# Optimization experiments

Measured on AMD Instinct MI355X. Metric: run time of the kernel, lower is better.

## Reference

```python
import jax, jax.numpy as jnp
import numpy as np
import math

B, S, D, H = 2, 2048, 1024, 16
HD = D // H  # head_dim = 64


def setup_inputs() -> dict:
    rng = jax.random.key(0)
    ks = jax.random.split(rng, 11)
    std = 1.0 / math.sqrt(D)
    inp = {
        "query": jax.random.normal(ks[0], (B, S, D), dtype=jnp.float32),
        "key": jax.random.normal(ks[1], (B, S, D), dtype=jnp.float32),
        "value": jax.random.normal(ks[2], (B, S, D), dtype=jnp.float32),
        # causal mask: True = masked (ignored), matching masked_fill semantics
        "mask": jnp.triu(jnp.ones((S, S), dtype=bool), k=1),
        "wq": jax.random.normal(ks[3], (D, D), dtype=jnp.float32) * std,
        "bq": jnp.zeros((D,), dtype=jnp.float32),
        "wk": jax.random.normal(ks[4], (D, D), dtype=jnp.float32) * std,
        "bk": jnp.zeros((D,), dtype=jnp.float32),
        "wv": jax.random.normal(ks[5], (D, D), dtype=jnp.float32) * std,
        "bv": jnp.zeros((D,), dtype=jnp.float32),
        "wo": jax.random.normal(ks[6], (D, D), dtype=jnp.float32) * std,
        "bo": jnp.zeros((D,), dtype=jnp.float32),
    }
    return inp


def reference(query, key, value, mask, wq, bq, wk, bk, wv, bv, wo, bo):
    # Linear projections (torch Linear: x @ W.T + b)
    q = jnp.einsum('bsd,ed->bse', query, wq) + bq
    k = jnp.einsum('bsd,ed->bse', key, wk) + bk
    v = jnp.einsum('bsd,ed->bse', value, wv) + bv
    # split heads: (B, S, D) -> (B, H, S, HD)
    q = q.reshape(B, S, H, HD).transpose(0, 2, 1, 3)
    k = k.reshape(B, S, H, HD).transpose(0, 2, 1, 3)
    v = v.reshape(B, S, H, HD).transpose(0, 2, 1, 3)
    # naive attention: materialize full (B, H, Sq, Sk) scores
    scores = jnp.einsum('bhqd,bhkd->bhqk', q, k) / jnp.sqrt(jnp.float32(HD))
    scores = jnp.where(mask[None, None, :, :], -jnp.inf, scores)
    attn = jax.nn.softmax(scores, axis=-1)
    out = jnp.einsum('bhqk,bhkd->bhqd', attn, v)
    out = out.transpose(0, 2, 1, 3).reshape(B, S, D)
    return jnp.einsum('bsd,ed->bse', out, wo) + bo
```

## Files before the change

kernel.cpp:

```cpp
#include <hip/hip_runtime.h>
#include <stdint.h>

#define B_ 2
#define S_ 2048
#define D_ 1024
#define H_ 16
#define HD_ 64
#define M_TOT (B_*S_)

typedef __bf16 bf16;
typedef bf16 bf16x8 __attribute__((ext_vector_type(8)));
typedef float f32x4 __attribute__((ext_vector_type(4)));
typedef float f32x16 __attribute__((ext_vector_type(16)));
typedef unsigned int u32;
typedef unsigned int u32x4v __attribute__((ext_vector_type(4)));

__device__ __forceinline__ void gload_lds16(const void* g, void* l) {
    __builtin_amdgcn_global_load_lds((const __attribute__((address_space(1))) void*)g,
                                     (__attribute__((address_space(3))) void*)l, 16, 0, 0);
}

__device__ __forceinline__ u32 cvtpk_bf16(float lo, float hi) {
    u32 d;
    asm("v_cvt_pk_bf16_f32 %0, %1, %2" : "=v"(d) : "v"(lo), "v"(hi));
    return d;
}

__global__ __launch_bounds__(256) void cvt_kernel(
    const float* __restrict__ q, const float* __restrict__ k, const float* __restrict__ v,
    const float* __restrict__ wq, const float* __restrict__ wk,
    const float* __restrict__ wv, const float* __restrict__ wo,
    bf16* __restrict__ xq, bf16* __restrict__ xk, bf16* __restrict__ xv,
    bf16* __restrict__ wqb, bf16* __restrict__ wkb, bf16* __restrict__ wvb, bf16* __restrict__ wob)
{
    const float* src; bf16* dst; int n;
    switch (blockIdx.y) {
        case 0: src=q;  dst=xq;  n=M_TOT*D_; break;
        case 1: src=k;  dst=xk;  n=M_TOT*D_; break;
        case 2: src=v;  dst=xv;  n=M_TOT*D_; break;
        case 3: src=wq; dst=wqb; n=D_*D_;    break;
        case 4: src=wk; dst=wkb; n=D_*D_;    break;
        case 5: src=wv; dst=wvb; n=D_*D_;    break;
        default: src=wo; dst=wob; n=D_*D_;   break;
    }
    int i = (blockIdx.x*blockDim.x + threadIdx.x)*8;
    if (i >= n) return;
    const f32x4* s4 = (const f32x4*)(src + i);
    f32x4 a = s4[0], b = s4[1];
    bf16x8 o;
    #pragma unroll
    for (int j = 0; j < 4; ++j) { o[j] = (bf16)a[j]; o[j+4] = (bf16)b[j]; }
    *(bf16x8*)(dst + i) = o;
}

__device__ __forceinline__ void gemm_mainloop(const bf16* __restrict__ A, const bf16* __restrict__ Wt,
                                              int brow, int bcol, bf16* As, bf16* Bs,
                                              f32x4 (&acc)[4][4])
{
    const int tid = threadIdx.x;
    const int l = tid & 63, w = tid >> 6;
    const int wr = w >> 1, wc = w & 1;
    const int lr = l & 15, lq = l >> 4;

    for (int k0 = 0; k0 < D_; k0 += 32) {
        #pragma unroll
        for (int i = 0; i < 2; ++i) {
            int id = i*256 + tid;
            int row = id >> 2, c8 = (id & 3) << 3;
            gload_lds16(A  + (size_t)(brow + row)*D_ + k0 + c8, As + id*8);
            gload_lds16(Wt + (size_t)(bcol + row)*D_ + k0 + c8, Bs + id*8);
        }
        __syncthreads();
        bf16x8 af[4], bf[4];
        #pragma unroll
        for (int m = 0; m < 4; ++m)
            af[m] = *(const bf16x8*)&As[(wr*64 + m*16 + lr)*32 + lq*8];
        #pragma unroll
        for (int n = 0; n < 4; ++n)
            bf[n] = *(const bf16x8*)&Bs[(wc*64 + n*16 + lr)*32 + lq*8];
        #pragma unroll
        for (int m = 0; m < 4; ++m)
            #pragma unroll
            for (int n = 0; n < 4; ++n)
                acc[m][n] = __builtin_amdgcn_mfma_f32_16x16x32_bf16(af[m], bf[n], acc[m][n], 0, 0, 0);
        __syncthreads();
    }
}

__global__ __launch_bounds__(256) void gemm_qkv(
    const bf16* __restrict__ xq, const bf16* __restrict__ xk, const bf16* __restrict__ xv,
    const bf16* __restrict__ wqb, const bf16* __restrict__ wkb, const bf16* __restrict__ wvb,
    const float* __restrict__ bq, const float* __restrict__ bk, const float* __restrict__ bv,
    bf16* __restrict__ Qf, bf16* __restrict__ Kf, bf16* __restrict__ Vf)
{
    __shared__ __align__(16) bf16 As[128*32];
    __shared__ __align__(16) bf16 Bs[128*32];
    const int z = blockIdx.z;
    const bf16* A  = (z==0) ? xq  : (z==1) ? xk  : xv;
    const bf16* Wt = (z==0) ? wqb : (z==1) ? wkb : wvb;
    const float* bias = (z==0) ? bq : (z==1) ? bk : bv;

    const int brow = (blockIdx.x & 31)*128;
    const int bcol = (blockIdx.x >> 5)*128;

    f32x4 acc[4][4] = {};
    gemm_mainloop(A, Wt, brow, bcol, As, Bs, acc);

    const int tid = threadIdx.x;
    const int l = tid & 63, w = tid >> 6;
    const int wr = w >> 1, wc = w & 1;
    const int lr = l & 15, lq = l >> 4;

    #pragma unroll
    for (int m = 0; m < 4; ++m)
        #pragma unroll
        for (int n = 0; n < 4; ++n) {
            int col = bcol + wc*64 + n*16 + lr;
            float bv_ = bias[col];
            int h = col >> 6, hd = col & 63;
            #pragma unroll
            for (int r = 0; r < 4; ++r) {
                int row = brow + wr*64 + m*16 + lq*4 + r;
                int b = row >> 11, s = row & 2047;
                float val = acc[m][n][r] + bv_;
                if (z == 0) val *= 0.18033688011112042f;
                size_t hbase = ((size_t)b*H_ + h)*S_*HD_;
                if (z < 2) {
                    int chunk = ((s >> 5) << 2) + (hd >> 4);
                    int lane  = (((hd >> 3) & 1) << 5) | (s & 31);
                    bf16* dst = (z==0) ? Qf : Kf;
                    dst[hbase + (size_t)chunk*512 + lane*8 + (hd & 7)] = (bf16)val;
                } else {
                    int chunk = ((s >> 6) << 3) + (((s >> 4) & 3) << 1) + (hd >> 5);
                    int lane  = (((s >> 3) & 1) << 5) | (hd & 31);
                    Vf[hbase + (size_t)chunk*512 + lane*8 + (s & 7)] = (bf16)val;
                }
            }
        }
}

__global__ __launch_bounds__(256) void gemm_out(
    const bf16* __restrict__ Oat, const bf16* __restrict__ wob,
    const float* __restrict__ bo, float* __restrict__ out)
{
    __shared__ __align__(16) bf16 As[128*32];
    __shared__ __align__(16) bf16 Bs[128*32];
    const int brow = (blockIdx.x & 31)*128;
    const int bcol = (blockIdx.x >> 5)*128;

    f32x4 acc[4][4] = {};
    gemm_mainloop(Oat, wob, brow, bcol, As, Bs, acc);

    const int tid = threadIdx.x;
    const int l = tid & 63, w = tid >> 6;
    const int wr = w >> 1, wc = w & 1;
    const int lr = l & 15, lq = l >> 4;

    #pragma unroll
    for (int m = 0; m < 4; ++m)
        #pragma unroll
        for (int n = 0; n < 4; ++n) {
            int col = bcol + wc*64 + n*16 + lr;
            float bv_ = bo[col];
            #pragma unroll
            for (int r = 0; r < 4; ++r) {
                int row = brow + wr*64 + m*16 + lq*4 + r;
                out[(size_t)row*D_ + col] = acc[m][n][r] + bv_;
            }
        }
}

__global__ __launch_bounds__(64, 2) void attn_kernel(
    const bf16* __restrict__ Qf, const bf16* __restrict__ Kf,
    const bf16* __restrict__ Vf, bf16* __restrict__ Oat)
{
    __shared__ __align__(16) char Osm[32*128];

    const int l = threadIdx.x & 63;
    const int l31 = l & 31, hi = l >> 5;

    const int id = (int)blockIdx.x;
    const int xcd = id & 7, slot = id >> 3;
    const int bh  = xcd + 8*(slot >> 6);
    const int qt  = 63 - (slot & 63);
    const int b = bh >> 4, h = bh & 15;
    const int q0 = qt*32;
    const int qrow = q0 + l31;

    const bf16* Qfp = Qf + (size_t)bh*S_*HD_;
    const bf16* Kfp = Kf + (size_t)bh*S_*HD_;
    const bf16* Vfp = Vf + (size_t)bh*S_*HD_;
    const int l8 = l*8;

    bf16x8 qb[4];
    #pragma unroll
    for (int dc = 0; dc < 4; ++dc)
        qb[dc] = *(const bf16x8*)(Qfp + (size_t)(((q0 >> 5) << 2) + dc)*512 + l8);

    f32x16 ot0 = {}, ot1 = {};
    float mrun = -1e30f, lrun = 0.f;
    const int nkt = q0/64 + 1;

    bf16x8 ka[2][4];
    #pragma unroll
    for (int kv2 = 0; kv2 < 2; ++kv2)
        #pragma unroll
        for (int dc = 0; dc < 4; ++dc)
            ka[kv2][dc] = *(const bf16x8*)(Kfp + (size_t)(kv2*4 + dc)*512 + l8);

    for (int kt = 0; kt < nkt; ++kt) {
        const int kc0 = kt*64;
        const bool last = (kt == nkt - 1);

        const int ktn = (kt + 1 < nkt) ? kt + 1 : kt;
        bf16x8 kn[2][4];
        #pragma unroll
        for (int kv2 = 0; kv2 < 2; ++kv2)
            #pragma unroll
            for (int dc = 0; dc < 4; ++dc)
                kn[kv2][dc] = *(const bf16x8*)(Kfp + (size_t)((ktn*2 + kv2)*4 + dc)*512 + l8);
        bf16x8 va0[4], va1[4];
        #pragma unroll
        for (int c = 0; c < 4; ++c) {
            va0[c] = *(const bf16x8*)(Vfp + (size_t)(kt*8 + c*2 + 0)*512 + l8);
            va1[c] = *(const bf16x8*)(Vfp + (size_t)(kt*8 + c*2 + 1)*512 + l8);
        }

        f32x16 ct0 = {}, ct1 = {};
        #pragma unroll
        for (int dc = 0; dc < 4; ++dc)
            ct0 = __builtin_amdgcn_mfma_f32_32x32x16_bf16(ka[0][dc], qb[dc], ct0, 0, 0, 0);
        #pragma unroll
        for (int dc = 0; dc < 4; ++dc)
            ct1 = __builtin_amdgcn_mfma_f32_32x32x16_bf16(ka[1][dc], qb[dc], ct1, 0, 0, 0);

        if (last) {
            #pragma unroll
            for (int reg = 0; reg < 16; ++reg) {
                const int rr = (reg & 3) + 8*(reg >> 2) + 4*hi;
                if (kc0 + rr > qrow)      ct0[reg] = -1e30f;
                if (kc0 + 32 + rr > qrow) ct1[reg] = -1e30f;
            }
        }

        float t8[8];
        #pragma unroll
        for (int i = 0; i < 8; ++i)
            t8[i] = fmaxf(fmaxf(ct0[i], ct0[i+8]), fmaxf(ct1[i], ct1[i+8]));
        float t4a = fmaxf(t8[0], t8[4]), t4b = fmaxf(t8[1], t8[5]);
        float t4c = fmaxf(t8[2], t8[6]), t4d = fmaxf(t8[3], t8[7]);
        float vm = fmaxf(fmaxf(t4a, t4b), fmaxf(t4c, t4d));
        vm = fmaxf(vm, __shfl_xor(vm, 32));

        if (!__all(vm <= mrun + 8.f)) {
            float nm = fmaxf(mrun, vm);
            float al = exp2f(mrun - nm);
            #pragma unroll
            for (int i = 0; i < 16; ++i) { ot0[i] *= al; ot1[i] *= al; }
            lrun *= al;
            mrun = nm;
        }

        #pragma unroll
        for (int i = 0; i < 16; ++i) {
            ct0[i] = exp2f(ct0[i] - mrun);
            ct1[i] = exp2f(ct1[i] - mrun);
        }
        float s8[8];
        #pragma unroll
        for (int i = 0; i < 8; ++i)
            s8[i] = (ct0[i] + ct0[i+8]) + (ct1[i] + ct1[i+8]);
        float s4a = s8[0]+s8[4], s4b = s8[1]+s8[5], s4c = s8[2]+s8[6], s4d = s8[3]+s8[7];
        float ps = (s4a + s4b) + (s4c + s4d);
        ps += __shfl_xor(ps, 32);
        lrun += ps;

        u32 own0[8], own1[8], oth0[8], oth1[8];
        #pragma unroll
        for (int u = 0; u < 8; ++u) {
            own0[u] = cvtpk_bf16(ct0[2*u], ct0[2*u+1]);
            own1[u] = cvtpk_bf16(ct1[2*u], ct1[2*u+1]);
        }
        #pragma unroll
        for (int u = 0; u < 8; ++u) {
            oth0[u] = __shfl_xor(own0[u], 32);
            oth1[u] = __shfl_xor(own1[u], 32);
        }

        #pragma unroll
        for (int c = 0; c < 4; ++c) {
            const int b0 = 4*(c & 1);
            const u32* Ho = (c >> 1) ? own1 : own0;
            const u32* Hx = (c >> 1) ? oth1 : oth0;
            u32 w0 = hi ? Hx[b0+2] : Ho[b0];
            u32 w1 = hi ? Hx[b0+3] : Ho[b0+1];
            u32 w2 = hi ? Ho[b0+2] : Hx[b0];
            u32 w3 = hi ? Ho[b0+3] : Hx[b0+1];
            u32x4v pw = { w0, w1, w2, w3 };
            bf16x8 pb = __builtin_bit_cast(bf16x8, pw);
            ot0 = __builtin_amdgcn_mfma_f32_32x32x16_bf16(va0[c], pb, ot0, 0, 0, 0);
            ot1 = __builtin_amdgcn_mfma_f32_32x32x16_bf16(va1[c], pb, ot1, 0, 0, 0);
        }

        #pragma unroll
        for (int kv2 = 0; kv2 < 2; ++kv2)
            #pragma unroll
            for (int dc = 0; dc < 4; ++dc)
                ka[kv2][dc] = kn[kv2][dc];
    }

    const float inv = 1.f / lrun;
    #pragma unroll
    for (int rp = 0; rp < 16; rp += 2) {
        const int d0 = (rp & 3) + 8*(rp >> 2) + 4*hi;
        u32 p0 = cvtpk_bf16(ot0[rp]*inv, ot0[rp+1]*inv);
        u32 p1 = cvtpk_bf16(ot1[rp]*inv, ot1[rp+1]*inv);
        const int swz = (l31 & 7) << 4;
        *(u32*)(Osm + l31*128 + (( d0*2)        ^ swz)) = p0;
        *(u32*)(Osm + l31*128 + (((32 + d0)*2)  ^ swz)) = p1;
    }
    #pragma unroll
    for (int p = 0; p < 4; ++p) {
        const int row  = p*8 + (l >> 3);
        const int colb = (l & 7)*16;
        u32x4v v = *(const u32x4v*)(Osm + row*128 + (colb ^ ((row & 7) << 4)));
        char* gp = (char*)Oat + (((size_t)(b*S_ + q0 + row)*D_ + h*64)*2) + colb;
        *(u32x4v*)gp = v;
    }
}

extern "C" void kernel_launch(void* const* d_in, const int* in_sizes, int n_in,
                              void* d_out, int out_size, void* d_ws, size_t ws_size,
                              hipStream_t stream) {
    const float* q  = (const float*)d_in[0];
    const float* k  = (const float*)d_in[1];
    const float* v  = (const float*)d_in[2];
    const float* wq = (const float*)d_in[4];
    const float* bq = (const float*)d_in[5];
    const float* wk = (const float*)d_in[6];
    const float* bk = (const float*)d_in[7];
    const float* wv = (const float*)d_in[8];
    const float* bv = (const float*)d_in[9];
    const float* wo = (const float*)d_in[10];
    const float* bo = (const float*)d_in[11];
    float* out = (float*)d_out;

    char* p = (char*)d_ws;
    const size_t XSZ = (size_t)M_TOT*D_*sizeof(bf16);
    const size_t WSZ = (size_t)D_*D_*sizeof(bf16);
    bf16* xq  = (bf16*)p; p += XSZ;
    bf16* xk  = (bf16*)p; p += XSZ;
    bf16* xv  = (bf16*)p; p += XSZ;
    bf16* wqb = (bf16*)p; p += WSZ;
    bf16* wkb = (bf16*)p; p += WSZ;
    bf16* wvb = (bf16*)p; p += WSZ;
    bf16* wob = (bf16*)p; p += WSZ;
    bf16* Qf  = (bf16*)p; p += XSZ;
    bf16* Kf  = (bf16*)p; p += XSZ;
    bf16* Vf  = (bf16*)p; p += XSZ;
    bf16* Oat = (bf16*)p; p += XSZ;

    cvt_kernel<<<dim3(2048, 7), 256, 0, stream>>>(q, k, v, wq, wk, wv, wo,
                                                  xq, xk, xv, wqb, wkb, wvb, wob);
    gemm_qkv<<<dim3(256, 1, 3), 256, 0, stream>>>(xq, xk, xv, wqb, wkb, wvb,
                                                  bq, bk, bv, Qf, Kf, Vf);
    attn_kernel<<<2048, 64, 0, stream>>>(Qf, Kf, Vf, Oat);
    gemm_out<<<dim3(256), 256, 0, stream>>>(Oat, wob, bo, out);
}
```

Before: 140.3 us.

## Unroll attention KV loop by two with ping-pong K registers and reorder q-tile schedule

The attention key loop is manually unrolled by two through a macro, alternating two K register buffers so the prefetched next tile does not need a copy back into the current buffer. P-fragment selection is rewritten with explicit branches instead of pointer selection, which helps keep the arrays in registers. The q-tile to block mapping is also changed: the causal tile order is interleaved and half the slots run in ascending order, which mixes long and short blocks within each scheduling group. Both K buffers are live at once, which may raise register pressure, and the new block order could change L2 locality.

```diff
diff --git a/kernel.cpp b/kernel.cpp
--- a/kernel.cpp
+++ b/kernel.cpp
@@ -170,6 +170,98 @@
         }
 }
 
+#define ATTN_BODY(CUR, NXT, KT) do {                                                        \
+    const int kc0_ = (KT)*64;                                                               \
+    const bool last_ = ((KT) == nkt - 1);                                                   \
+    const int ktn_ = ((KT) + 1 < nkt) ? (KT) + 1 : (KT);                                    \
+    _Pragma("unroll")                                                                       \
+    for (int kv2 = 0; kv2 < 2; ++kv2)                                                       \
+        _Pragma("unroll")                                                                   \
+        for (int dc = 0; dc < 4; ++dc)                                                      \
+            NXT[kv2][dc] = *(const bf16x8*)(Kfp + (size_t)((ktn_*2 + kv2)*4 + dc)*512 + l8);\
+    bf16x8 va0[4], va1[4];                                                                  \
+    _Pragma("unroll")                                                                       \
+    for (int c = 0; c < 4; ++c) {                                                           \
+        va0[c] = *(const bf16x8*)(Vfp + (size_t)((KT)*8 + c*2 + 0)*512 + l8);               \
+        va1[c] = *(const bf16x8*)(Vfp + (size_t)((KT)*8 + c*2 + 1)*512 + l8);               \
+    }                                                                                       \
+    f32x16 ct0 = {}, ct1 = {};                                                              \
+    _Pragma("unroll")                                                                       \
+    for (int dc = 0; dc < 4; ++dc)                                                          \
+        ct0 = __builtin_amdgcn_mfma_f32_32x32x16_bf16(CUR[0][dc], qb[dc], ct0, 0, 0, 0);    \
+    _Pragma("unroll")                                                                       \
+    for (int dc = 0; dc < 4; ++dc)                                                          \
+        ct1 = __builtin_amdgcn_mfma_f32_32x32x16_bf16(CUR[1][dc], qb[dc], ct1, 0, 0, 0);    \
+    if (last_) {                                                                            \
+        _Pragma("unroll")                                                                   \
+        for (int reg = 0; reg < 16; ++reg) {                                                \
+            const int rr = (reg & 3) + 8*(reg >> 2) + 4*hi;                                 \
+            if (kc0_ + rr > qrow)      ct0[reg] = -1e30f;                                   \
+            if (kc0_ + 32 + rr > qrow) ct1[reg] = -1e30f;                                   \
+        }                                                                                   \
+    }                                                                                       \
+    float t8[8];                                                                            \
+    _Pragma("unroll")                                                                       \
+    for (int i = 0; i < 8; ++i)                                                             \
+        t8[i] = fmaxf(fmaxf(ct0[i], ct0[i+8]), fmaxf(ct1[i], ct1[i+8]));                    \
+    float t4a = fmaxf(t8[0], t8[4]), t4b = fmaxf(t8[1], t8[5]);                             \
+    float t4c = fmaxf(t8[2], t8[6]), t4d = fmaxf(t8[3], t8[7]);                             \
+    float vm = fmaxf(fmaxf(t4a, t4b), fmaxf(t4c, t4d));                                     \
+    vm = fmaxf(vm, __shfl_xor(vm, 32));                                                     \
+    if (!__all(vm <= mrun + 8.f)) {                                                         \
+        float nm = fmaxf(mrun, vm);                                                         \
+        float al = exp2f(mrun - nm);                                                        \
+        _Pragma("unroll")                                                                   \
+        for (int i = 0; i < 16; ++i) { ot0[i] *= al; ot1[i] *= al; }                        \
+        lrun *= al;                                                                         \
+        mrun = nm;                                                                          \
+    }                                                                                       \
+    _Pragma("unroll")                                                                       \
+    for (int i = 0; i < 16; ++i) {                                                          \
+        ct0[i] = exp2f(ct0[i] - mrun);                                                      \
+        ct1[i] = exp2f(ct1[i] - mrun);                                                      \
+    }                                                                                       \
+    float s8[8];                                                                            \
+    _Pragma("unroll")                                                                       \
+    for (int i = 0; i < 8; ++i)                                                             \
+        s8[i] = (ct0[i] + ct0[i+8]) + (ct1[i] + ct1[i+8]);                                  \
+    float s4a = s8[0]+s8[4], s4b = s8[1]+s8[5], s4c = s8[2]+s8[6], s4d = s8[3]+s8[7];       \
+    float ps = (s4a + s4b) + (s4c + s4d);                                                   \
+    ps += __shfl_xor(ps, 32);                                                               \
+    lrun += ps;                                                                             \
+    u32 own0[8], own1[8], oth0[8], oth1[8];                                                 \
+    _Pragma("unroll")                                                                       \
+    for (int u = 0; u < 8; ++u) {                                                           \
+        own0[u] = cvtpk_bf16(ct0[2*u], ct0[2*u+1]);                                         \
+        own1[u] = cvtpk_bf16(ct1[2*u], ct1[2*u+1]);                                         \
+    }                                                                                       \
+    _Pragma("unroll")                                                                       \
+    for (int u = 0; u < 8; ++u) {                                                           \
+        oth0[u] = __shfl_xor(own0[u], 32);                                                  \
+        oth1[u] = __shfl_xor(own1[u], 32);                                                  \
+    }                                                                                       \
+    _Pragma("unroll")                                                                       \
+    for (int c = 0; c < 4; ++c) {                                                           \
+        const int b0 = 4*(c & 1);                                                           \
+        u32 o0, o1, o2, o3, x0, x1, x2, x3;                                                 \
+        if ((c >> 1) == 0) {                                                                \
+            o0 = own0[b0]; o1 = own0[b0+1]; o2 = own0[b0+2]; o3 = own0[b0+3];               \
+            x0 = oth0[b0]; x1 = oth0[b0+1]; x2 = oth0[b0+2]; x3 = oth0[b0+3];               \
+        } else {                                                                            \
+            o0 = own1[b0]; o1 = own1[b0+1]; o2 = own1[b0+2]; o3 = own1[b0+3];               \
+            x0 = oth1[b0]; x1 = oth1[b0+1]; x2 = oth1[b0+2]; x3 = oth1[b0+3];               \
+        }                                                                                   \
+        u32 w0 = hi ? x2 : o0;                                                              \
+        u32 w1 = hi ? x3 : o1;                                                              \
+        u32 w2 = hi ? o2 : x0;                                                              \
+        u32 w3 = hi ? o3 : x1;                                                              \
+        u32x4v pw = { w0, w1, w2, w3 };                                                     \
+        bf16x8 pb = __builtin_bit_cast(bf16x8, pw);                                         \
+        ot0 = __builtin_amdgcn_mfma_f32_32x32x16_bf16(va0[c], pb, ot0, 0, 0, 0);            \
+        ot1 = __builtin_amdgcn_mfma_f32_32x32x16_bf16(va1[c], pb, ot1, 0, 0, 0);            \
+    }                                                                                       \
+} while (0)
+
 __global__ __launch_bounds__(64, 2) void attn_kernel(
     const bf16* __restrict__ Qf, const bf16* __restrict__ Kf,
     const bf16* __restrict__ Vf, bf16* __restrict__ Oat)
@@ -182,7 +274,10 @@
     const int id = (int)blockIdx.x;
     const int xcd = id & 7, slot = id >> 3;
     const int bh  = xcd + 8*(slot >> 6);
-    const int qt  = 63 - (slot & 63);
+    const int s6 = slot & 63;
+    const int sb = s6 & 31;
+    const int g  = ((sb & 7) << 3) | (sb >> 3);
+    const int qt = (s6 < 32) ? g : 63 - g;
     const int b = bh >> 4, h = bh & 15;
     const int q0 = qt*32;
     const int qrow = q0 + l31;
@@ -201,112 +296,20 @@
     float mrun = -1e30f, lrun = 0.f;
     const int nkt = q0/64 + 1;
 
-    bf16x8 ka[2][4];
+    bf16x8 ka[2][4], kb[2][4];
     #pragma unroll
     for (int kv2 = 0; kv2 < 2; ++kv2)
         #pragma unroll
         for (int dc = 0; dc < 4; ++dc)
             ka[kv2][dc] = *(const bf16x8*)(Kfp + (size_t)(kv2*4 + dc)*512 + l8);
 
-    for (int kt = 0; kt < nkt; ++kt) {
-        const int kc0 = kt*64;
-        const bool last = (kt == nkt - 1);
-
-        const int ktn = (kt + 1 < nkt) ? kt + 1 : kt;
-        bf16x8 kn[2][4];
-        #pragma unroll
-        for (int kv2 = 0; kv2 < 2; ++kv2)
-            #pragma unroll
-            for (int dc = 0; dc < 4; ++dc)
-                kn[kv2][dc] = *(const bf16x8*)(Kfp + (size_t)((ktn*2 + kv2)*4 + dc)*512 + l8);
-        bf16x8 va0[4], va1[4];
-        #pragma unroll
-        for (int c = 0; c < 4; ++c) {
-            va0[c] = *(const bf16x8*)(Vfp + (size_t)(kt*8 + c*2 + 0)*512 + l8);
-            va1[c] = *(const bf16x8*)(Vfp + (size_t)(kt*8 + c*2 + 1)*512 + l8);
-        }
-
-        f32x16 ct0 = {}, ct1 = {};
-        #pragma unroll
-        for (int dc = 0; dc < 4; ++dc)
-            ct0 = __builtin_amdgcn_mfma_f32_32x32x16_bf16(ka[0][dc], qb[dc], ct0, 0, 0, 0);
-        #pragma unroll
-        for (int dc = 0; dc < 4; ++dc)
-            ct1 = __builtin_amdgcn_mfma_f32_32x32x16_bf16(ka[1][dc], qb[dc], ct1, 0, 0, 0);
-
-        if (last) {
-            #pragma unroll
-            for (int reg = 0; reg < 16; ++reg) {
-                const int rr = (reg & 3) + 8*(reg >> 2) + 4*hi;
-                if (kc0 + rr > qrow)      ct0[reg] = -1e30f;
-                if (kc0 + 32 + rr > qrow) ct1[reg] = -1e30f;
-            }
-        }
-
-        float t8[8];
-        #pragma unroll
-        for (int i = 0; i < 8; ++i)
-            t8[i] = fmaxf(fmaxf(ct0[i], ct0[i+8]), fmaxf(ct1[i], ct1[i+8]));
-        float t4a = fmaxf(t8[0], t8[4]), t4b = fmaxf(t8[1], t8[5]);
-        float t4c = fmaxf(t8[2], t8[6]), t4d = fmaxf(t8[3], t8[7]);
-        float vm = fmaxf(fmaxf(t4a, t4b), fmaxf(t4c, t4d));
-        vm = fmaxf(vm, __shfl_xor(vm, 32));
-
-        if (!__all(vm <= mrun + 8.f)) {
-            float nm = fmaxf(mrun, vm);
-            float al = exp2f(mrun - nm);
-            #pragma unroll
-            for (int i = 0; i < 16; ++i) { ot0[i] *= al; ot1[i] *= al; }
-            lrun *= al;
-            mrun = nm;
-        }
-
-        #pragma unroll
-        for (int i = 0; i < 16; ++i) {
-            ct0[i] = exp2f(ct0[i] - mrun);
-            ct1[i] = exp2f(ct1[i] - mrun);
-        }
-        float s8[8];
-        #pragma unroll
-        for (int i = 0; i < 8; ++i)
-            s8[i] = (ct0[i] + ct0[i+8]) + (ct1[i] + ct1[i+8]);
-        float s4a = s8[0]+s8[4], s4b = s8[1]+s8[5], s4c = s8[2]+s8[6], s4d = s8[3]+s8[7];
-        float ps = (s4a + s4b) + (s4c + s4d);
-        ps += __shfl_xor(ps, 32);
-        lrun += ps;
-
-        u32 own0[8], own1[8], oth0[8], oth1[8];
-        #pragma unroll
-        for (int u = 0; u < 8; ++u) {
-            own0[u] = cvtpk_bf16(ct0[2*u], ct0[2*u+1]);
-            own1[u] = cvtpk_bf16(ct1[2*u], ct1[2*u+1]);
-        }
-        #pragma unroll
-        for (int u = 0; u < 8; ++u) {
-            oth0[u] = __shfl_xor(own0[u], 32);
-            oth1[u] = __shfl_xor(own1[u], 32);
-        }
-
-        #pragma unroll
-        for (int c = 0; c < 4; ++c) {
-            const int b0 = 4*(c & 1);
-            const u32* Ho = (c >> 1) ? own1 : own0;
-            const u32* Hx = (c >> 1) ? oth1 : oth0;
-            u32 w0 = hi ? Hx[b0+2] : Ho[b0];
-            u32 w1 = hi ? Hx[b0+3] : Ho[b0+1];
-            u32 w2 = hi ? Ho[b0+2] : Hx[b0];
-            u32 w3 = hi ? Ho[b0+3] : Hx[b0+1];
-            u32x4v pw = { w0, w1, w2, w3 };
-            bf16x8 pb = __builtin_bit_cast(bf16x8, pw);
-            ot0 = __builtin_amdgcn_mfma_f32_32x32x16_bf16(va0[c], pb, ot0, 0, 0, 0);
-            ot1 = __builtin_amdgcn_mfma_f32_32x32x16_bf16(va1[c], pb, ot1, 0, 0, 0);
-        }
-
-        #pragma unroll
-        for (int kv2 = 0; kv2 < 2; ++kv2)
-            #pragma unroll
-            for (int dc = 0; dc < 4; ++dc)
-                ka[kv2][dc] = kn[kv2][dc];
+    int kt = 0;
+    while (kt + 1 < nkt) {
+        ATTN_BODY(ka, kb, kt); ++kt;
+        ATTN_BODY(kb, ka, kt); ++kt;
+    }
+    if (kt < nkt) {
+        ATTN_BODY(ka, kb, kt);
     }
 
     const float inv = 1.f / lrun;
```

Result: no change. 139.6 us (-0.5%).
